# Optimization experiments

Hardware: AMD Instinct MI355X
Metric: run time of the kernel (lower is better)

Reference implementation:

```python
import jax, jax.numpy as jnp
import numpy as np

TOP_K = 2
NORM_TOPK = True


def setup_inputs() -> dict:
    key = jax.random.key(0)
    k1, k2, k3, k4 = jax.random.split(key, 4)
    B, S, H = 2, 1024, 2048
    E, I = 16, 768
    hidden_states = jax.random.normal(k1, (B, S, H), dtype=jnp.float32)
    gate_w = jax.random.normal(k2, (E, H), dtype=jnp.float32) * 0.02
    gate_up_w = jax.random.normal(k3, (E, 2 * I, H), dtype=jnp.float32) * 0.02
    down_w = jax.random.normal(k4, (E, H, I), dtype=jnp.float32) * 0.02
    return {
        "hidden_states": hidden_states,
        "gate_w": gate_w,
        "gate_up_w": gate_up_w,
        "down_w": down_w,
        "top_k": TOP_K,
    }


def reference(hidden_states, gate_w, gate_up_w, down_w, top_k):
    B, S, H = hidden_states.shape
    E = gate_w.shape[0]
    x = hidden_states.reshape(-1, H)  # [T, H]
    T = x.shape[0]

    # Router: softmax in float32 (as in torch F.softmax(..., dtype=torch.float))
    router_logits = x @ gate_w.T  # [T, E]
    probs = jax.nn.softmax(router_logits.astype(jnp.float32), axis=-1)
    top_w, top_idx = jax.lax.top_k(probs, top_k)  # [T, k]
    if NORM_TOPK:
        top_w = top_w / jnp.sum(top_w, axis=-1, keepdims=True)
    top_w = top_w.astype(x.dtype)

    # Dense combine weights [T, E]: routing weight where selected, 0 elsewhere.
    comb = jnp.sum(jax.nn.one_hot(top_idx, E, dtype=x.dtype) * top_w[..., None], axis=1)

    # SwiGLU expert MLPs evaluated for all experts, combined with sparse weights.
    gu = jnp.einsum("th,efh->tef", x, gate_up_w)  # [T, E, 2I]
    g, u = jnp.split(gu, 2, axis=-1)
    h = jax.nn.silu(g) * u  # [T, E, I]
    y = jnp.einsum("tei,ehi->teh", h, down_w)  # [T, E, H]
    out = jnp.einsum("teh,te->th", y, comb)  # [T, H]

    return out.reshape(B, S, H), router_logits
```

## Files before the change

kernel.cpp:

```cpp
#include <hip/hip_runtime.h>
#include <hip/hip_bf16.h>
#include <stdint.h>

#define T_TOK 2048
#define H_DIM 2048
#define E_NUM 16
#define I_DIM 768

typedef __bf16 bf16;
typedef __bf16 bf16x4 __attribute__((ext_vector_type(4)));
typedef __bf16 bf16x8 __attribute__((ext_vector_type(8)));
typedef float f32x4 __attribute__((ext_vector_type(4)));

__device__ __forceinline__ void async_cp16(void* l, const void* g) {
    __builtin_amdgcn_global_load_lds(
        (const __attribute__((address_space(1))) void*)g,
        (__attribute__((address_space(3))) void*)l, 16, 0, 0);
}

__global__ __launch_bounds__(256) void router_kernel(
    const float* __restrict__ x, const float* __restrict__ gw,
    float* __restrict__ logits, int* __restrict__ cnt,
    int* __restrict__ tok_list, float* __restrict__ wgt_list,
    bf16* __restrict__ xb)
{
    const int t = blockIdx.x;
    const int tid = threadIdx.x;
    const int lane = tid & 63, wid = tid >> 6;

    double part[E_NUM];
#pragma unroll
    for (int e = 0; e < E_NUM; ++e) part[e] = 0.0;

#pragma unroll
    for (int it = 0; it < 2; ++it) {
        int h = it * 1024 + tid * 4;
        float4 xv = *(const float4*)(x + (size_t)t * H_DIM + h);
        bf16x4 xb4 = { (bf16)xv.x, (bf16)xv.y, (bf16)xv.z, (bf16)xv.w };
        *(bf16x4*)(xb + (size_t)t * H_DIM + h) = xb4;
#pragma unroll
        for (int e = 0; e < E_NUM; ++e) {
            float4 wv = *(const float4*)(gw + (size_t)e * H_DIM + h);
            part[e] += (double)xv.x * (double)wv.x + (double)xv.y * (double)wv.y
                     + (double)xv.z * (double)wv.z + (double)xv.w * (double)wv.w;
        }
    }
#pragma unroll
    for (int off = 32; off > 0; off >>= 1)
#pragma unroll
        for (int e = 0; e < E_NUM; ++e)
            part[e] += __shfl_down(part[e], off);

    __shared__ double sh[4][E_NUM];
    __shared__ float lg[E_NUM];
    if (lane == 0)
#pragma unroll
        for (int e = 0; e < E_NUM; ++e) sh[wid][e] = part[e];
    __syncthreads();
    if (tid < E_NUM) {
        float v = (float)(sh[0][tid] + sh[1][tid] + sh[2][tid] + sh[3][tid]);
        lg[tid] = v;
        logits[(size_t)t * E_NUM + tid] = v;
    }
    __syncthreads();
    if (tid == 0) {
        int i0 = 0; float v0 = lg[0];
#pragma unroll
        for (int e = 1; e < E_NUM; ++e) if (lg[e] > v0) { v0 = lg[e]; i0 = e; }
        int i1 = -1; float v1 = -3.4e38f;
#pragma unroll
        for (int e = 0; e < E_NUM; ++e) if (e != i0 && lg[e] > v1) { v1 = lg[e]; i1 = e; }
        float w0 = 1.0f / (1.0f + __expf(v1 - v0));
        float w1 = 1.0f - w0;
        int p0 = atomicAdd(&cnt[i0], 1);
        tok_list[i0 * T_TOK + p0] = t; wgt_list[i0 * T_TOK + p0] = w0;
        int p1 = atomicAdd(&cnt[i1], 1);
        tok_list[i1 * T_TOK + p1] = t; wgt_list[i1 * T_TOK + p1] = w1;
    }
}

__global__ void scan_kernel(const int* __restrict__ cnt, int* __restrict__ offs)
{
    if (threadIdx.x == 0) {
        int o = 0;
        for (int e = 0; e < E_NUM; ++e) { offs[e] = o; o += cnt[e]; }
    }
}

__global__ __launch_bounds__(256, 4) void gateup_kernel(
    const bf16* __restrict__ xb, const float* __restrict__ gup,
    const int* __restrict__ cnt, const int* __restrict__ offs,
    const int* __restrict__ tok_list, bf16* __restrict__ hbuf)
{
    const int e = blockIdx.z;
    const int count = cnt[e];
    const int row0 = blockIdx.y * 64;
    if (row0 >= count) return;
    const int i0 = blockIdx.x * 64;
    const int hoff = offs[e];
    const int tid = threadIdx.x;
    const int lane = tid & 63, wid = tid >> 6;

    __shared__ __align__(16) bf16 As[64 * 64];
    __shared__ __align__(16) float Bs[128 * 64];

    int raA0 = tid >> 3, sA0 = tid & 7;
    int raA1 = raA0 + 32;
    int cA0 = sA0 ^ (raA0 & 7);
    int cA1 = sA0 ^ (raA1 & 7);
    int tr0 = row0 + raA0; if (tr0 >= count) tr0 = count - 1;
    int tr1 = row0 + raA1; if (tr1 >= count) tr1 = count - 1;
    const bf16* srcA0 = xb + (size_t)tok_list[e * T_TOK + tr0] * H_DIM + cA0 * 8;
    const bf16* srcA1 = xb + (size_t)tok_list[e * T_TOK + tr1] * H_DIM + cA1 * 8;
    bf16* dstA0 = As + (size_t)(wid * 64) * 8;
    bf16* dstA1 = As + (size_t)(wid * 64 + 256) * 8;

    const float* srcB[8]; float* dstB[8];
#pragma unroll
    for (int i = 0; i < 8; ++i) {
        int idx = i * 256 + tid;
        int r = idx >> 4, s = idx & 15;
        int c = s ^ (r & 15);
        int is_u = (r >> 5) & 1;
        int ioff = (r >> 6) * 32 + (r & 31);
        size_t grow = (size_t)e * (2 * I_DIM) + (size_t)is_u * I_DIM + i0 + ioff;
        srcB[i] = gup + grow * H_DIM + c * 4;
        dstB[i] = Bs + (size_t)(i * 256 + wid * 64) * 4;
    }

    f32x4 acc[2][4];
#pragma unroll
    for (int a = 0; a < 2; ++a)
#pragma unroll
        for (int b = 0; b < 4; ++b) acc[a][b] = (f32x4){0.f, 0.f, 0.f, 0.f};

    const int la = lane & 15, lq = lane >> 4;
    const int wm = wid >> 1, wn = wid & 1;

    for (int k0 = 0; k0 < H_DIM; k0 += 64) {
        async_cp16(dstA0, srcA0 + k0);
        async_cp16(dstA1, srcA1 + k0);
#pragma unroll
        for (int i = 0; i < 8; ++i) async_cp16(dstB[i], srcB[i] + k0);
        __syncthreads();
#pragma unroll
        for (int ks = 0; ks < 2; ++ks) {
            bf16x8 af[2], bfr[4];
            int chA = ks * 4 + lq;
            int c0 = ks * 8 + lq * 2;
#pragma unroll
            for (int mt = 0; mt < 2; ++mt) {
                int row = 32 * wm + 16 * mt + la;
                int sl = chA ^ (row & 7);
                af[mt] = *(const bf16x8*)(As + (size_t)(row * 8 + sl) * 8);
            }
#pragma unroll
            for (int nt = 0; nt < 4; ++nt) {
                int row = 64 * wn + 16 * nt + la;
                int s0 = c0 ^ (row & 15);
                int s1 = s0 ^ 1;
                f32x4 v0 = *(const f32x4*)(Bs + (size_t)(row * 16 + s0) * 4);
                f32x4 v1 = *(const f32x4*)(Bs + (size_t)(row * 16 + s1) * 4);
                bfr[nt] = (bf16x8){ (bf16)v0.x, (bf16)v0.y, (bf16)v0.z, (bf16)v0.w,
                                    (bf16)v1.x, (bf16)v1.y, (bf16)v1.z, (bf16)v1.w };
            }
#pragma unroll
            for (int mt = 0; mt < 2; ++mt)
#pragma unroll
                for (int nt = 0; nt < 4; ++nt)
                    acc[mt][nt] = __builtin_amdgcn_mfma_f32_16x16x32_bf16(af[mt], bfr[nt], acc[mt][nt], 0, 0, 0);
        }
        __syncthreads();
    }

#pragma unroll
    for (int mt = 0; mt < 2; ++mt)
#pragma unroll
        for (int p = 0; p < 2; ++p)
#pragma unroll
            for (int r = 0; r < 4; ++r) {
                int trow = 32 * wm + 16 * mt + lq * 4 + r;
                if (row0 + trow < count) {
                    float g = acc[mt][p][r], u = acc[mt][p + 2][r];
                    float hv = (g / (1.0f + __expf(-g))) * u;
                    int col = i0 + 32 * wn + 16 * p + la;
                    hbuf[(size_t)(hoff + row0 + trow) * I_DIM + col] = (bf16)hv;
                }
            }
}

__global__ __launch_bounds__(256, 4) void down_kernel(
    const float* __restrict__ dw, const bf16* __restrict__ hbuf,
    const int* __restrict__ cnt, const int* __restrict__ offs,
    const int* __restrict__ tok_list, const float* __restrict__ wgt_list,
    float* __restrict__ out)
{
    const int e = blockIdx.z;
    const int count = cnt[e];
    const int row0 = blockIdx.y * 64;
    if (row0 >= count) return;
    const int n0 = blockIdx.x * 128;
    const int hoff = offs[e];
    const int tid = threadIdx.x;
    const int lane = tid & 63, wid = tid >> 6;

    __shared__ __align__(16) bf16 As[64 * 64];
    __shared__ __align__(16) float Bs[128 * 64];

    int raA0 = tid >> 3, sA0 = tid & 7;
    int raA1 = raA0 + 32;
    int cA0 = sA0 ^ (raA0 & 7);
    int cA1 = sA0 ^ (raA1 & 7);
    int ar0 = row0 + raA0; if (ar0 >= count) ar0 = count - 1;
    int ar1 = row0 + raA1; if (ar1 >= count) ar1 = count - 1;
    const bf16* srcA0 = hbuf + (size_t)(hoff + ar0) * I_DIM + cA0 * 8;
    const bf16* srcA1 = hbuf + (size_t)(hoff + ar1) * I_DIM + cA1 * 8;
    bf16* dstA0 = As + (size_t)(wid * 64) * 8;
    bf16* dstA1 = As + (size_t)(wid * 64 + 256) * 8;

    const float* srcB[8]; float* dstB[8];
#pragma unroll
    for (int i = 0; i < 8; ++i) {
        int idx = i * 256 + tid;
        int r = idx >> 4, s = idx & 15;
        int c = s ^ (r & 15);
        srcB[i] = dw + ((size_t)e * H_DIM + n0 + r) * I_DIM + c * 4;
        dstB[i] = Bs + (size_t)(i * 256 + wid * 64) * 4;
    }

    f32x4 acc[2][4];
#pragma unroll
    for (int a = 0; a < 2; ++a)
#pragma unroll
        for (int b = 0; b < 4; ++b) acc[a][b] = (f32x4){0.f, 0.f, 0.f, 0.f};

    const int la = lane & 15, lq = lane >> 4;
    const int wm = wid >> 1, wn = wid & 1;

    for (int k0 = 0; k0 < I_DIM; k0 += 64) {
        async_cp16(dstA0, srcA0 + k0);
        async_cp16(dstA1, srcA1 + k0);
#pragma unroll
        for (int i = 0; i < 8; ++i) async_cp16(dstB[i], srcB[i] + k0);
        __syncthreads();
#pragma unroll
        for (int ks = 0; ks < 2; ++ks) {
            bf16x8 af[2], bfr[4];
            int chA = ks * 4 + lq;
            int c0 = ks * 8 + lq * 2;
#pragma unroll
            for (int mt = 0; mt < 2; ++mt) {
                int row = 32 * wm + 16 * mt + la;
                int sl = chA ^ (row & 7);
                af[mt] = *(const bf16x8*)(As + (size_t)(row * 8 + sl) * 8);
            }
#pragma unroll
            for (int nt = 0; nt < 4; ++nt) {
                int row = 64 * wn + 16 * nt + la;
                int s0 = c0 ^ (row & 15);
                int s1 = s0 ^ 1;
                f32x4 v0 = *(const f32x4*)(Bs + (size_t)(row * 16 + s0) * 4);
                f32x4 v1 = *(const f32x4*)(Bs + (size_t)(row * 16 + s1) * 4);
                bfr[nt] = (bf16x8){ (bf16)v0.x, (bf16)v0.y, (bf16)v0.z, (bf16)v0.w,
                                    (bf16)v1.x, (bf16)v1.y, (bf16)v1.z, (bf16)v1.w };
            }
#pragma unroll
            for (int mt = 0; mt < 2; ++mt)
#pragma unroll
                for (int nt = 0; nt < 4; ++nt)
                    acc[mt][nt] = __builtin_amdgcn_mfma_f32_16x16x32_bf16(af[mt], bfr[nt], acc[mt][nt], 0, 0, 0);
        }
        __syncthreads();
    }

#pragma unroll
    for (int mt = 0; mt < 2; ++mt)
#pragma unroll
        for (int nt = 0; nt < 4; ++nt)
#pragma unroll
            for (int r = 0; r < 4; ++r) {
                int trow = 32 * wm + 16 * mt + lq * 4 + r;
                if (row0 + trow < count) {
                    int col = n0 + 64 * wn + 16 * nt + la;
                    int grow = row0 + trow;
                    atomicAdd(&out[(size_t)tok_list[e * T_TOK + grow] * H_DIM + col],
                              wgt_list[e * T_TOK + grow] * acc[mt][nt][r]);
                }
            }
}

extern "C" void kernel_launch(void* const* d_in, const int* in_sizes, int n_in,
                              void* d_out, int out_size, void* d_ws, size_t ws_size,
                              hipStream_t stream)
{
    const float* x   = (const float*)d_in[0];
    const float* gw  = (const float*)d_in[1];
    const float* gup = (const float*)d_in[2];
    const float* dw  = (const float*)d_in[3];
    float* out = (float*)d_out;
    float* logits = out + (size_t)T_TOK * H_DIM;

    char* ws = (char*)d_ws;
    int*   cnt      = (int*)(ws + 0);
    int*   offs     = (int*)(ws + 256);
    int*   tok_list = (int*)(ws + 512);
    float* wgt_list = (float*)(ws + 131584);
    bf16*  hbuf     = (bf16*)(ws + 262656);
    bf16*  xb       = (bf16*)(ws + 6554112);

    hipMemsetAsync(cnt, 0, 256, stream);
    hipMemsetAsync(out, 0, (size_t)T_TOK * H_DIM * sizeof(float), stream);

    router_kernel<<<T_TOK, 256, 0, stream>>>(x, gw, logits, cnt, tok_list, wgt_list, xb);
    scan_kernel<<<1, 64, 0, stream>>>(cnt, offs);
    gateup_kernel<<<dim3(I_DIM / 64, T_TOK / 64, E_NUM), 256, 0, stream>>>(
        xb, gup, cnt, offs, tok_list, hbuf);
    down_kernel<<<dim3(H_DIM / 128, T_TOK / 64, E_NUM), 256, 0, stream>>>(
        dw, hbuf, cnt, offs, tok_list, wgt_list, out);
}
```

Measured before the change: 529.2 us.

## Double-buffer LDS tiles in gate-up and down expert GEMM kernels

Both expert GEMM kernels now keep two LDS buffers for the A and B tiles. The loads for the next K-tile are issued before the current tile is computed, so global-to-LDS transfer overlaps with MFMA work and the barrier between load and compute is removed. This doubles LDS per block to about 80KB, and launch bounds drop from 4 to 2 blocks per CU. The trade-off is that lower occupancy can reduce latency hiding across blocks.

```diff
diff --git a/kernel.cpp b/kernel.cpp
--- a/kernel.cpp
+++ b/kernel.cpp
@@ -87,7 +87,7 @@
     }
 }
 
-__global__ __launch_bounds__(256, 4) void gateup_kernel(
+__global__ __launch_bounds__(256, 2) void gateup_kernel(
     const bf16* __restrict__ xb, const float* __restrict__ gup,
     const int* __restrict__ cnt, const int* __restrict__ offs,
     const int* __restrict__ tok_list, bf16* __restrict__ hbuf)
@@ -101,8 +101,8 @@
     const int tid = threadIdx.x;
     const int lane = tid & 63, wid = tid >> 6;
 
-    __shared__ __align__(16) bf16 As[64 * 64];
-    __shared__ __align__(16) float Bs[128 * 64];
+    __shared__ __align__(16) bf16 As[2][64 * 64];
+    __shared__ __align__(16) float Bs[2][128 * 64];
 
     int raA0 = tid >> 3, sA0 = tid & 7;
     int raA1 = raA0 + 32;
@@ -112,10 +112,10 @@
     int tr1 = row0 + raA1; if (tr1 >= count) tr1 = count - 1;
     const bf16* srcA0 = xb + (size_t)tok_list[e * T_TOK + tr0] * H_DIM + cA0 * 8;
     const bf16* srcA1 = xb + (size_t)tok_list[e * T_TOK + tr1] * H_DIM + cA1 * 8;
-    bf16* dstA0 = As + (size_t)(wid * 64) * 8;
-    bf16* dstA1 = As + (size_t)(wid * 64 + 256) * 8;
-
-    const float* srcB[8]; float* dstB[8];
+    const int dA0 = (wid * 64) * 8;
+    const int dA1 = (wid * 64 + 256) * 8;
+
+    const float* srcB[8]; int dB[8];
 #pragma unroll
     for (int i = 0; i < 8; ++i) {
         int idx = i * 256 + tid;
@@ -125,7 +125,7 @@
         int ioff = (r >> 6) * 32 + (r & 31);
         size_t grow = (size_t)e * (2 * I_DIM) + (size_t)is_u * I_DIM + i0 + ioff;
         srcB[i] = gup + grow * H_DIM + c * 4;
-        dstB[i] = Bs + (size_t)(i * 256 + wid * 64) * 4;
+        dB[i] = (i * 256 + wid * 64) * 4;
     }
 
     f32x4 acc[2][4];
@@ -137,12 +137,20 @@
     const int la = lane & 15, lq = lane >> 4;
     const int wm = wid >> 1, wn = wid & 1;
 
+    auto stage = [&](int buf, int k0) {
+        async_cp16(&As[buf][dA0], srcA0 + k0);
+        async_cp16(&As[buf][dA1], srcA1 + k0);
+#pragma unroll
+        for (int i = 0; i < 8; ++i) async_cp16(&Bs[buf][dB[i]], srcB[i] + k0);
+    };
+
+    stage(0, 0);
+    __syncthreads();
+    int cur = 0;
     for (int k0 = 0; k0 < H_DIM; k0 += 64) {
-        async_cp16(dstA0, srcA0 + k0);
-        async_cp16(dstA1, srcA1 + k0);
-#pragma unroll
-        for (int i = 0; i < 8; ++i) async_cp16(dstB[i], srcB[i] + k0);
-        __syncthreads();
+        if (k0 + 64 < H_DIM) stage(cur ^ 1, k0 + 64);
+        const bf16* Asc = As[cur];
+        const float* Bsc = Bs[cur];
 #pragma unroll
         for (int ks = 0; ks < 2; ++ks) {
             bf16x8 af[2], bfr[4];
@@ -152,15 +160,15 @@
             for (int mt = 0; mt < 2; ++mt) {
                 int row = 32 * wm + 16 * mt + la;
                 int sl = chA ^ (row & 7);
-                af[mt] = *(const bf16x8*)(As + (size_t)(row * 8 + sl) * 8);
+                af[mt] = *(const bf16x8*)(Asc + (size_t)(row * 8 + sl) * 8);
             }
 #pragma unroll
             for (int nt = 0; nt < 4; ++nt) {
                 int row = 64 * wn + 16 * nt + la;
                 int s0 = c0 ^ (row & 15);
                 int s1 = s0 ^ 1;
-                f32x4 v0 = *(const f32x4*)(Bs + (size_t)(row * 16 + s0) * 4);
-                f32x4 v1 = *(const f32x4*)(Bs + (size_t)(row * 16 + s1) * 4);
+                f32x4 v0 = *(const f32x4*)(Bsc + (size_t)(row * 16 + s0) * 4);
+                f32x4 v1 = *(const f32x4*)(Bsc + (size_t)(row * 16 + s1) * 4);
                 bfr[nt] = (bf16x8){ (bf16)v0.x, (bf16)v0.y, (bf16)v0.z, (bf16)v0.w,
                                     (bf16)v1.x, (bf16)v1.y, (bf16)v1.z, (bf16)v1.w };
             }
@@ -171,6 +179,7 @@
                     acc[mt][nt] = __builtin_amdgcn_mfma_f32_16x16x32_bf16(af[mt], bfr[nt], acc[mt][nt], 0, 0, 0);
         }
         __syncthreads();
+        cur ^= 1;
     }
 
 #pragma unroll
@@ -189,7 +198,7 @@
             }
 }
 
-__global__ __launch_bounds__(256, 4) void down_kernel(
+__global__ __launch_bounds__(256, 2) void down_kernel(
     const float* __restrict__ dw, const bf16* __restrict__ hbuf,
     const int* __restrict__ cnt, const int* __restrict__ offs,
     const int* __restrict__ tok_list, const float* __restrict__ wgt_list,
@@ -204,8 +213,8 @@
     const int tid = threadIdx.x;
     const int lane = tid & 63, wid = tid >> 6;
 
-    __shared__ __align__(16) bf16 As[64 * 64];
-    __shared__ __align__(16) float Bs[128 * 64];
+    __shared__ __align__(16) bf16 As[2][64 * 64];
+    __shared__ __align__(16) float Bs[2][128 * 64];
 
     int raA0 = tid >> 3, sA0 = tid & 7;
     int raA1 = raA0 + 32;
@@ -215,17 +224,17 @@
     int ar1 = row0 + raA1; if (ar1 >= count) ar1 = count - 1;
     const bf16* srcA0 = hbuf + (size_t)(hoff + ar0) * I_DIM + cA0 * 8;
     const bf16* srcA1 = hbuf + (size_t)(hoff + ar1) * I_DIM + cA1 * 8;
-    bf16* dstA0 = As + (size_t)(wid * 64) * 8;
-    bf16* dstA1 = As + (size_t)(wid * 64 + 256) * 8;
-
-    const float* srcB[8]; float* dstB[8];
+    const int dA0 = (wid * 64) * 8;
+    const int dA1 = (wid * 64 + 256) * 8;
+
+    const float* srcB[8]; int dB[8];
 #pragma unroll
     for (int i = 0; i < 8; ++i) {
         int idx = i * 256 + tid;
         int r = idx >> 4, s = idx & 15;
         int c = s ^ (r & 15);
         srcB[i] = dw + ((size_t)e * H_DIM + n0 + r) * I_DIM + c * 4;
-        dstB[i] = Bs + (size_t)(i * 256 + wid * 64) * 4;
+        dB[i] = (i * 256 + wid * 64) * 4;
     }
 
     f32x4 acc[2][4];
@@ -237,12 +246,20 @@
     const int la = lane & 15, lq = lane >> 4;
     const int wm = wid >> 1, wn = wid & 1;
 
+    auto stage = [&](int buf, int k0) {
+        async_cp16(&As[buf][dA0], srcA0 + k0);
+        async_cp16(&As[buf][dA1], srcA1 + k0);
+#pragma unroll
+        for (int i = 0; i < 8; ++i) async_cp16(&Bs[buf][dB[i]], srcB[i] + k0);
+    };
+
+    stage(0, 0);
+    __syncthreads();
+    int cur = 0;
     for (int k0 = 0; k0 < I_DIM; k0 += 64) {
-        async_cp16(dstA0, srcA0 + k0);
-        async_cp16(dstA1, srcA1 + k0);
-#pragma unroll
-        for (int i = 0; i < 8; ++i) async_cp16(dstB[i], srcB[i] + k0);
-        __syncthreads();
+        if (k0 + 64 < I_DIM) stage(cur ^ 1, k0 + 64);
+        const bf16* Asc = As[cur];
+        const float* Bsc = Bs[cur];
 #pragma unroll
         for (int ks = 0; ks < 2; ++ks) {
             bf16x8 af[2], bfr[4];
@@ -252,15 +269,15 @@
             for (int mt = 0; mt < 2; ++mt) {
                 int row = 32 * wm + 16 * mt + la;
                 int sl = chA ^ (row & 7);
-                af[mt] = *(const bf16x8*)(As + (size_t)(row * 8 + sl) * 8);
+                af[mt] = *(const bf16x8*)(Asc + (size_t)(row * 8 + sl) * 8);
             }
 #pragma unroll
             for (int nt = 0; nt < 4; ++nt) {
                 int row = 64 * wn + 16 * nt + la;
                 int s0 = c0 ^ (row & 15);
                 int s1 = s0 ^ 1;
-                f32x4 v0 = *(const f32x4*)(Bs + (size_t)(row * 16 + s0) * 4);
-                f32x4 v1 = *(const f32x4*)(Bs + (size_t)(row * 16 + s1) * 4);
+                f32x4 v0 = *(const f32x4*)(Bsc + (size_t)(row * 16 + s0) * 4);
+                f32x4 v1 = *(const f32x4*)(Bsc + (size_t)(row * 16 + s1) * 4);
                 bfr[nt] = (bf16x8){ (bf16)v0.x, (bf16)v0.y, (bf16)v0.z, (bf16)v0.w,
                                     (bf16)v1.x, (bf16)v1.y, (bf16)v1.z, (bf16)v1.w };
             }
@@ -271,6 +288,7 @@
                     acc[mt][nt] = __builtin_amdgcn_mfma_f32_16x16x32_bf16(af[mt], bfr[nt], acc[mt][nt], 0, 0, 0);
         }
         __syncthreads();
+        cur ^= 1;
     }
 
 #pragma unroll
```

New measurement: 545.7 us. 1.03x slower.

## Replace LDS staging with direct register double-buffered global loads in expert GEMMs

Applied to the files above, without the earlier changes.

Both expert GEMM kernels stop staging tiles through LDS with async copies and barriers. Each lane now loads its MFMA operand fragments straight from global memory into registers, double-buffered so the next K tile's loads are issued before the current tile is computed. Launch bounds drop to 2 waves per SIMD to make room for the larger register footprint. This removes LDS traffic and the per-tile __syncthreads, but each wave loses cross-wave data sharing, so global and L2 reads of the weight and activation tiles go up, and occupancy is lower.

```diff
diff --git a/kernel.cpp b/kernel.cpp
--- a/kernel.cpp
+++ b/kernel.cpp
@@ -11,12 +11,6 @@
 typedef __bf16 bf16x4 __attribute__((ext_vector_type(4)));
 typedef __bf16 bf16x8 __attribute__((ext_vector_type(8)));
 typedef float f32x4 __attribute__((ext_vector_type(4)));
-
-__device__ __forceinline__ void async_cp16(void* l, const void* g) {
-    __builtin_amdgcn_global_load_lds(
-        (const __attribute__((address_space(1))) void*)g,
-        (__attribute__((address_space(3))) void*)l, 16, 0, 0);
-}
 
 __global__ __launch_bounds__(256) void router_kernel(
     const float* __restrict__ x, const float* __restrict__ gw,
@@ -87,7 +81,7 @@
     }
 }
 
-__global__ __launch_bounds__(256, 4) void gateup_kernel(
+__global__ __launch_bounds__(256, 2) void gateup_kernel(
     const bf16* __restrict__ xb, const float* __restrict__ gup,
     const int* __restrict__ cnt, const int* __restrict__ offs,
     const int* __restrict__ tok_list, bf16* __restrict__ hbuf)
@@ -100,67 +94,54 @@
     const int hoff = offs[e];
     const int tid = threadIdx.x;
     const int lane = tid & 63, wid = tid >> 6;
-
-    __shared__ __align__(16) bf16 As[64 * 64];
-    __shared__ __align__(16) float Bs[128 * 64];
-
-    int raA0 = tid >> 3, sA0 = tid & 7;
-    int raA1 = raA0 + 32;
-    int cA0 = sA0 ^ (raA0 & 7);
-    int cA1 = sA0 ^ (raA1 & 7);
-    int tr0 = row0 + raA0; if (tr0 >= count) tr0 = count - 1;
-    int tr1 = row0 + raA1; if (tr1 >= count) tr1 = count - 1;
-    const bf16* srcA0 = xb + (size_t)tok_list[e * T_TOK + tr0] * H_DIM + cA0 * 8;
-    const bf16* srcA1 = xb + (size_t)tok_list[e * T_TOK + tr1] * H_DIM + cA1 * 8;
-    bf16* dstA0 = As + (size_t)(wid * 64) * 8;
-    bf16* dstA1 = As + (size_t)(wid * 64 + 256) * 8;
-
-    const float* srcB[8]; float* dstB[8];
-#pragma unroll
-    for (int i = 0; i < 8; ++i) {
-        int idx = i * 256 + tid;
-        int r = idx >> 4, s = idx & 15;
-        int c = s ^ (r & 15);
-        int is_u = (r >> 5) & 1;
-        int ioff = (r >> 6) * 32 + (r & 31);
-        size_t grow = (size_t)e * (2 * I_DIM) + (size_t)is_u * I_DIM + i0 + ioff;
-        srcB[i] = gup + grow * H_DIM + c * 4;
-        dstB[i] = Bs + (size_t)(i * 256 + wid * 64) * 4;
-    }
-
-    f32x4 acc[2][4];
-#pragma unroll
-    for (int a = 0; a < 2; ++a)
-#pragma unroll
-        for (int b = 0; b < 4; ++b) acc[a][b] = (f32x4){0.f, 0.f, 0.f, 0.f};
-
     const int la = lane & 15, lq = lane >> 4;
     const int wm = wid >> 1, wn = wid & 1;
 
-    for (int k0 = 0; k0 < H_DIM; k0 += 64) {
-        async_cp16(dstA0, srcA0 + k0);
-        async_cp16(dstA1, srcA1 + k0);
-#pragma unroll
-        for (int i = 0; i < 8; ++i) async_cp16(dstB[i], srcB[i] + k0);
-        __syncthreads();
+    const bf16* srcA[2];
+#pragma unroll
+    for (int mt = 0; mt < 2; ++mt) {
+        int tr = row0 + 32 * wm + 16 * mt + la;
+        if (tr >= count) tr = count - 1;
+        srcA[mt] = xb + (size_t)tok_list[e * T_TOK + tr] * H_DIM + lq * 8;
+    }
+    const float* srcB[4];
+#pragma unroll
+    for (int nt = 0; nt < 4; ++nt) {
+        size_t grow = (size_t)e * (2 * I_DIM) + (size_t)(nt >> 1) * I_DIM
+                    + i0 + 32 * wn + 16 * (nt & 1) + la;
+        srcB[nt] = gup + grow * H_DIM + lq * 8;
+    }
+
+    f32x4 acc[2][4];
+#pragma unroll
+    for (int a = 0; a < 2; ++a)
+#pragma unroll
+        for (int b = 0; b < 4; ++b) acc[a][b] = (f32x4){0.f, 0.f, 0.f, 0.f};
+
+    f32x4 vb0[4][4], vb1[4][4];
+    bf16x8 va0[2][2], va1[2][2];
+
+    auto loadT = [&](f32x4 (&vb)[4][4], bf16x8 (&va)[2][2], int k0) {
+#pragma unroll
+        for (int nt = 0; nt < 4; ++nt)
+#pragma unroll
+            for (int ks = 0; ks < 2; ++ks) {
+                vb[nt][ks * 2]     = *(const f32x4*)(srcB[nt] + k0 + ks * 32);
+                vb[nt][ks * 2 + 1] = *(const f32x4*)(srcB[nt] + k0 + ks * 32 + 4);
+            }
+#pragma unroll
+        for (int mt = 0; mt < 2; ++mt)
+#pragma unroll
+            for (int ks = 0; ks < 2; ++ks)
+                va[mt][ks] = *(const bf16x8*)(srcA[mt] + k0 + ks * 32);
+    };
+    auto computeT = [&](const f32x4 (&vb)[4][4], const bf16x8 (&va)[2][2]) {
 #pragma unroll
         for (int ks = 0; ks < 2; ++ks) {
-            bf16x8 af[2], bfr[4];
-            int chA = ks * 4 + lq;
-            int c0 = ks * 8 + lq * 2;
-#pragma unroll
-            for (int mt = 0; mt < 2; ++mt) {
-                int row = 32 * wm + 16 * mt + la;
-                int sl = chA ^ (row & 7);
-                af[mt] = *(const bf16x8*)(As + (size_t)(row * 8 + sl) * 8);
-            }
+            bf16x8 bfr[4];
 #pragma unroll
             for (int nt = 0; nt < 4; ++nt) {
-                int row = 64 * wn + 16 * nt + la;
-                int s0 = c0 ^ (row & 15);
-                int s1 = s0 ^ 1;
-                f32x4 v0 = *(const f32x4*)(Bs + (size_t)(row * 16 + s0) * 4);
-                f32x4 v1 = *(const f32x4*)(Bs + (size_t)(row * 16 + s1) * 4);
+                const f32x4 v0 = vb[nt][ks * 2], v1 = vb[nt][ks * 2 + 1];
                 bfr[nt] = (bf16x8){ (bf16)v0.x, (bf16)v0.y, (bf16)v0.z, (bf16)v0.w,
                                     (bf16)v1.x, (bf16)v1.y, (bf16)v1.z, (bf16)v1.w };
             }
@@ -168,9 +149,18 @@
             for (int mt = 0; mt < 2; ++mt)
 #pragma unroll
                 for (int nt = 0; nt < 4; ++nt)
-                    acc[mt][nt] = __builtin_amdgcn_mfma_f32_16x16x32_bf16(af[mt], bfr[nt], acc[mt][nt], 0, 0, 0);
+                    acc[mt][nt] = __builtin_amdgcn_mfma_f32_16x16x32_bf16(
+                        va[mt][ks], bfr[nt], acc[mt][nt], 0, 0, 0);
         }
-        __syncthreads();
+    };
+
+    const int NK = H_DIM / 64;
+    loadT(vb0, va0, 0);
+    for (int kt = 0; kt < NK; kt += 2) {
+        loadT(vb1, va1, (kt + 1) * 64);
+        computeT(vb0, va0);
+        if (kt + 2 < NK) loadT(vb0, va0, (kt + 2) * 64);
+        computeT(vb1, va1);
     }
 
 #pragma unroll
@@ -189,7 +179,7 @@
             }
 }
 
-__global__ __launch_bounds__(256, 4) void down_kernel(
+__global__ __launch_bounds__(256, 2) void down_kernel(
     const float* __restrict__ dw, const bf16* __restrict__ hbuf,
     const int* __restrict__ cnt, const int* __restrict__ offs,
     const int* __restrict__ tok_list, const float* __restrict__ wgt_list,
@@ -203,64 +193,53 @@
     const int hoff = offs[e];
     const int tid = threadIdx.x;
     const int lane = tid & 63, wid = tid >> 6;
-
-    __shared__ __align__(16) bf16 As[64 * 64];
-    __shared__ __align__(16) float Bs[128 * 64];
-
-    int raA0 = tid >> 3, sA0 = tid & 7;
-    int raA1 = raA0 + 32;
-    int cA0 = sA0 ^ (raA0 & 7);
-    int cA1 = sA0 ^ (raA1 & 7);
-    int ar0 = row0 + raA0; if (ar0 >= count) ar0 = count - 1;
-    int ar1 = row0 + raA1; if (ar1 >= count) ar1 = count - 1;
-    const bf16* srcA0 = hbuf + (size_t)(hoff + ar0) * I_DIM + cA0 * 8;
-    const bf16* srcA1 = hbuf + (size_t)(hoff + ar1) * I_DIM + cA1 * 8;
-    bf16* dstA0 = As + (size_t)(wid * 64) * 8;
-    bf16* dstA1 = As + (size_t)(wid * 64 + 256) * 8;
-
-    const float* srcB[8]; float* dstB[8];
-#pragma unroll
-    for (int i = 0; i < 8; ++i) {
-        int idx = i * 256 + tid;
-        int r = idx >> 4, s = idx & 15;
-        int c = s ^ (r & 15);
-        srcB[i] = dw + ((size_t)e * H_DIM + n0 + r) * I_DIM + c * 4;
-        dstB[i] = Bs + (size_t)(i * 256 + wid * 64) * 4;
-    }
-
-    f32x4 acc[2][4];
-#pragma unroll
-    for (int a = 0; a < 2; ++a)
-#pragma unroll
-        for (int b = 0; b < 4; ++b) acc[a][b] = (f32x4){0.f, 0.f, 0.f, 0.f};
-
     const int la = lane & 15, lq = lane >> 4;
     const int wm = wid >> 1, wn = wid & 1;
 
-    for (int k0 = 0; k0 < I_DIM; k0 += 64) {
-        async_cp16(dstA0, srcA0 + k0);
-        async_cp16(dstA1, srcA1 + k0);
-#pragma unroll
-        for (int i = 0; i < 8; ++i) async_cp16(dstB[i], srcB[i] + k0);
-        __syncthreads();
+    const bf16* srcA[2];
+#pragma unroll
+    for (int mt = 0; mt < 2; ++mt) {
+        int tr = row0 + 32 * wm + 16 * mt + la;
+        if (tr >= count) tr = count - 1;
+        srcA[mt] = hbuf + (size_t)(hoff + tr) * I_DIM + lq * 8;
+    }
+    const float* srcB[4];
+#pragma unroll
+    for (int nt = 0; nt < 4; ++nt) {
+        size_t grow = (size_t)e * H_DIM + n0 + 64 * wn + 16 * nt + la;
+        srcB[nt] = dw + grow * I_DIM + lq * 8;
+    }
+
+    f32x4 acc[2][4];
+#pragma unroll
+    for (int a = 0; a < 2; ++a)
+#pragma unroll
+        for (int b = 0; b < 4; ++b) acc[a][b] = (f32x4){0.f, 0.f, 0.f, 0.f};
+
+    f32x4 vb0[4][4], vb1[4][4];
+    bf16x8 va0[2][2], va1[2][2];
+
+    auto loadT = [&](f32x4 (&vb)[4][4], bf16x8 (&va)[2][2], int k0) {
+#pragma unroll
+        for (int nt = 0; nt < 4; ++nt)
+#pragma unroll
+            for (int ks = 0; ks < 2; ++ks) {
+                vb[nt][ks * 2]     = *(const f32x4*)(srcB[nt] + k0 + ks * 32);
+                vb[nt][ks * 2 + 1] = *(const f32x4*)(srcB[nt] + k0 + ks * 32 + 4);
+            }
+#pragma unroll
+        for (int mt = 0; mt < 2; ++mt)
+#pragma unroll
+            for (int ks = 0; ks < 2; ++ks)
+                va[mt][ks] = *(const bf16x8*)(srcA[mt] + k0 + ks * 32);
+    };
+    auto computeT = [&](const f32x4 (&vb)[4][4], const bf16x8 (&va)[2][2]) {
 #pragma unroll
         for (int ks = 0; ks < 2; ++ks) {
-            bf16x8 af[2], bfr[4];
-            int chA = ks * 4 + lq;
-            int c0 = ks * 8 + lq * 2;
-#pragma unroll
-            for (int mt = 0; mt < 2; ++mt) {
-                int row = 32 * wm + 16 * mt + la;
-                int sl = chA ^ (row & 7);
-                af[mt] = *(const bf16x8*)(As + (size_t)(row * 8 + sl) * 8);
-            }
+            bf16x8 bfr[4];
 #pragma unroll
             for (int nt = 0; nt < 4; ++nt) {
-                int row = 64 * wn + 16 * nt + la;
-                int s0 = c0 ^ (row & 15);
-                int s1 = s0 ^ 1;
-                f32x4 v0 = *(const f32x4*)(Bs + (size_t)(row * 16 + s0) * 4);
-                f32x4 v1 = *(const f32x4*)(Bs + (size_t)(row * 16 + s1) * 4);
+                const f32x4 v0 = vb[nt][ks * 2], v1 = vb[nt][ks * 2 + 1];
                 bfr[nt] = (bf16x8){ (bf16)v0.x, (bf16)v0.y, (bf16)v0.z, (bf16)v0.w,
                                     (bf16)v1.x, (bf16)v1.y, (bf16)v1.z, (bf16)v1.w };
             }
@@ -268,9 +247,18 @@
             for (int mt = 0; mt < 2; ++mt)
 #pragma unroll
                 for (int nt = 0; nt < 4; ++nt)
-                    acc[mt][nt] = __builtin_amdgcn_mfma_f32_16x16x32_bf16(af[mt], bfr[nt], acc[mt][nt], 0, 0, 0);
+                    acc[mt][nt] = __builtin_amdgcn_mfma_f32_16x16x32_bf16(
+                        va[mt][ks], bfr[nt], acc[mt][nt], 0, 0, 0);
         }
-        __syncthreads();
+    };
+
+    const int NK = I_DIM / 64;
+    loadT(vb0, va0, 0);
+    for (int kt = 0; kt < NK; kt += 2) {
+        loadT(vb1, va1, (kt + 1) * 64);
+        computeT(vb0, va0);
+        if (kt + 2 < NK) loadT(vb0, va0, (kt + 2) * 64);
+        computeT(vb1, va1);
     }
 
 #pragma unroll
```

Result: slower. 806.6 us (+52.4%).
